# Performance work log

Hardware: AMD Instinct MI355X
Metric: run time of the kernel (lower is better)

## Reference

```python
import jax, jax.numpy as jnp
import numpy as np

B, S, D_IN, D_OUT, RANK, HBS, ABS = 4, 2048, 4096, 4096, 32, 128, 16


def _hadamard(n: int) -> np.ndarray:
    H = np.array([[1.0]], dtype=np.float64)
    while H.shape[0] < n:
        H = np.block([[H, H], [H, -H]])
    return (H / np.sqrt(n)).astype(np.float32)


def setup_inputs() -> dict:
    key = jax.random.key(0)
    ks = jax.random.split(key, 6)
    x = jax.random.normal(ks[0], (B, S, D_IN), dtype=jnp.float32)
    # random +/-1 sign vector (matches torch.randint(0,2)*2-1)
    S_in = (jax.random.randint(ks[1], (D_IN,), 0, 2) * 2 - 1).astype(jnp.float32)
    H_block = jnp.asarray(_hadamard(HBS))  # orthonormal block Hadamard
    w_quantized = jax.random.normal(ks[2], (D_OUT, D_IN), dtype=jnp.float32) * 0.02
    lora_a = jax.random.normal(ks[3], (RANK, D_IN), dtype=jnp.float32) * 0.01
    lora_b = jax.random.normal(ks[4], (D_OUT, RANK), dtype=jnp.float32) * 0.01
    bias = jax.random.normal(ks[5], (D_OUT,), dtype=jnp.float32) * 0.01
    return {"x": x, "S_in": S_in, "H_block": H_block, "w_quantized": w_quantized,
            "lora_a": lora_a, "lora_b": lora_b, "bias": bias}


def _quantize_nvfp4(x, block_size=ABS):
    # per-block (size 16) NVFP4 fake-quant; numel here is divisible by block_size
    levels = jnp.array([0.0, 0.5, 1.0, 1.5, 2.0, 3.0, 4.0, 6.0], dtype=x.dtype)
    shape = x.shape
    xf = x.reshape(-1, block_size)
    amax = jnp.maximum(jnp.max(jnp.abs(xf), axis=-1, keepdims=True), 1e-12)
    scale = amax / 6.0
    x_norm = jnp.abs(xf) / scale
    idx = jnp.argmin(jnp.abs(x_norm[..., None] - levels), axis=-1)  # snap to grid
    xq = jnp.sign(xf) * levels[idx] * scale
    return xq.reshape(shape)


def _hadamard_rotate(x, S_in, H_block):
    # sign flip then block-diagonal Hadamard on the last dim
    shape = x.shape
    x_s = x * S_in
    x3 = x_s.reshape(*shape[:-1], shape[-1] // HBS, HBS)
    return (x3 @ H_block).reshape(shape)


def reference(x, S_in, H_block, w_quantized, lora_a, lora_b, bias):
    x_rot = _hadamard_rotate(x, S_in, H_block)          # [B,S,D_IN]
    x_q = _quantize_nvfp4(x_rot)                        # NVFP4 fake-quant activations
    out = jnp.einsum('bsd,od->bso', x_q, w_quantized)   # main GEMM
    # LoRA correction on the (unquantized) rotated activations
    out = out + jnp.einsum('bsr,or->bso', jnp.einsum('bsd,rd->bsr', x_rot, lora_a), lora_b)
    out = out + bias
    return out
```

## Files before the change

kernel.cpp:

```cpp
#include <hip/hip_runtime.h>

#define M_ROWS 8192
#define DIN    4096
#define DOUT   4096
#define RANK   32
#define KAUG   4128
#define KPAD   4160
#define KTILES 65
#define ROWS_PB 4
#define NROTB  (M_ROWS / ROWS_PB)

typedef __attribute__((ext_vector_type(8))) short short8;
typedef __attribute__((ext_vector_type(4))) float floatx4;

__device__ __forceinline__ unsigned short f2bf(float f) {
    unsigned int u = __float_as_uint(f);
    unsigned int r = (u + 0x7FFFu + ((u >> 16) & 1u)) >> 16;
    return (unsigned short)r;
}

__global__ __launch_bounds__(256) void prep_kernel(
    const float* __restrict__ x, const float* __restrict__ sgn,
    const float* __restrict__ lora_a,
    const float* __restrict__ w, const float* __restrict__ lora_b,
    unsigned short* __restrict__ xaug, unsigned short* __restrict__ waug)
{
    __shared__ unsigned short xrot[ROWS_PB][DIN];
    __shared__ float tred[ROWS_PB][RANK][8];

    const int t = threadIdx.x;

    if (blockIdx.x >= NROTB) {
        const int n = blockIdx.x - NROTB;
        unsigned short* wr = waug + (size_t)n * KPAD;
        const float* wsrc = w + (size_t)n * DIN;
        #pragma unroll
        for (int it = 0; it < 2; ++it) {
            const int base = (it * 256 + t) * 8;
            float4 a = ((const float4*)wsrc)[base >> 2];
            float4 b = ((const float4*)wsrc)[(base >> 2) + 1];
            unsigned int p0 = (unsigned int)f2bf(a.x) | ((unsigned int)f2bf(a.y) << 16);
            unsigned int p1 = (unsigned int)f2bf(a.z) | ((unsigned int)f2bf(a.w) << 16);
            unsigned int p2 = (unsigned int)f2bf(b.x) | ((unsigned int)f2bf(b.y) << 16);
            unsigned int p3 = (unsigned int)f2bf(b.z) | ((unsigned int)f2bf(b.w) << 16);
            *(uint4*)(wr + base) = make_uint4(p0, p1, p2, p3);
        }
        if (t < RANK)
            wr[DIN + t] = f2bf(lora_b[(size_t)n * RANK + t]);
        if (t < 4)
            *(uint4*)&wr[KAUG + t * 8] = make_uint4(0, 0, 0, 0);
        return;
    }

    const int row0 = blockIdx.x * ROWS_PB;
    const float inv = 0.08838834764831845f;

    float sg[16];
    #pragma unroll
    for (int q = 0; q < 4; ++q)
        *(float4*)&sg[4 * q] = ((const float4*)sgn)[t * 4 + q];

    if (t < ROWS_PB * 4) {
        const int rr = t >> 2, q = t & 3;
        *(uint4*)&xaug[(size_t)(row0 + rr) * KPAD + KAUG + q * 8] =
            make_uint4(0, 0, 0, 0);
    }

    #pragma unroll 1
    for (int rr = 0; rr < ROWS_PB; ++rr) {
        const float* xr = x + (size_t)(row0 + rr) * DIN;
        float v[16];
        #pragma unroll
        for (int q = 0; q < 4; ++q)
            *(float4*)&v[4 * q] = ((const float4*)xr)[t * 4 + q];
        #pragma unroll
        for (int j = 0; j < 16; ++j) v[j] *= sg[j];

        #pragma unroll
        for (int h = 1; h < 16; h <<= 1) {
            #pragma unroll
            for (int i = 0; i < 16; ++i) {
                if (!(i & h)) {
                    float a = v[i], b = v[i + h];
                    v[i] = a + b;
                    v[i + h] = a - b;
                }
            }
        }
        #pragma unroll
        for (int m = 1; m <= 4; m <<= 1) {
            const bool up = (t & m) != 0;
            #pragma unroll
            for (int j = 0; j < 16; ++j) {
                float o = __shfl_xor(v[j], m, 64);
                v[j] = up ? (o - v[j]) : (v[j] + o);
            }
        }
        #pragma unroll
        for (int j = 0; j < 16; ++j) v[j] *= inv;

        {
            unsigned int xp[8];
            #pragma unroll
            for (int j = 0; j < 8; ++j)
                xp[j] = (unsigned int)f2bf(v[2 * j]) |
                        ((unsigned int)f2bf(v[2 * j + 1]) << 16);
            *(uint4*)&xrot[rr][16 * t]     = make_uint4(xp[0], xp[1], xp[2], xp[3]);
            *(uint4*)&xrot[rr][16 * t + 8] = make_uint4(xp[4], xp[5], xp[6], xp[7]);
        }

        {
            float amax = 0.f;
            #pragma unroll
            for (int j = 0; j < 16; ++j) amax = fmaxf(amax, fabsf(v[j]));
            amax = fmaxf(amax, 1e-12f);
            float scale = amax / 6.0f;
            unsigned int pk[8];
            #pragma unroll
            for (int j = 0; j < 8; ++j) {
                unsigned short q2[2];
                #pragma unroll
                for (int e = 0; e < 2; ++e) {
                    float vv = v[2 * j + e];
                    float an = fabsf(vv) / scale;
                    float lev = 0.0f;
                    lev = an > 0.25f ? 0.5f : lev;
                    lev = an > 0.75f ? 1.0f : lev;
                    lev = an > 1.25f ? 1.5f : lev;
                    lev = an > 1.75f ? 2.0f : lev;
                    lev = an > 2.5f  ? 3.0f : lev;
                    lev = an > 3.5f  ? 4.0f : lev;
                    lev = an > 5.0f  ? 6.0f : lev;
                    q2[e] = f2bf(copysignf(lev * scale, vv));
                }
                pk[j] = (unsigned int)q2[0] | ((unsigned int)q2[1] << 16);
            }
            unsigned short* orow = xaug + (size_t)(row0 + rr) * KPAD + 16 * t;
            ((uint4*)orow)[0] = make_uint4(pk[0], pk[1], pk[2], pk[3]);
            ((uint4*)orow)[1] = make_uint4(pk[4], pk[5], pk[6], pk[7]);
        }
    }
    __syncthreads();

    {
        const int r = t >> 3, c = t & 7;
        const float* ar = lora_a + (size_t)r * DIN;
        float acc4[ROWS_PB] = {0.f, 0.f, 0.f, 0.f};
        #pragma unroll 1
        for (int i = 0; i < 64; ++i) {
            const int d = (c << 9) + (((i << 3) + (c << 3)) & 511);
            float4 a0 = *(const float4*)(ar + d);
            float4 a1 = *(const float4*)(ar + d + 4);
            #pragma unroll
            for (int rr = 0; rr < ROWS_PB; ++rr) {
                uint4 xb = *(const uint4*)&xrot[rr][d];
                float x0 = __uint_as_float(xb.x << 16);
                float x1 = __uint_as_float(xb.x & 0xFFFF0000u);
                float x2 = __uint_as_float(xb.y << 16);
                float x3 = __uint_as_float(xb.y & 0xFFFF0000u);
                float x4 = __uint_as_float(xb.z << 16);
                float x5 = __uint_as_float(xb.z & 0xFFFF0000u);
                float x6 = __uint_as_float(xb.w << 16);
                float x7 = __uint_as_float(xb.w & 0xFFFF0000u);
                acc4[rr] += a0.x * x0 + a0.y * x1 + a0.z * x2 + a0.w * x3 +
                            a1.x * x4 + a1.y * x5 + a1.z * x6 + a1.w * x7;
            }
        }
        #pragma unroll
        for (int rr = 0; rr < ROWS_PB; ++rr) tred[rr][r][c] = acc4[rr];
    }
    __syncthreads();
    if (t < ROWS_PB * RANK) {
        const int rr = t >> 5, rk = t & 31;
        float s = 0.f;
        #pragma unroll
        for (int k = 0; k < 8; ++k) s += tred[rr][rk][k];
        xaug[(size_t)(row0 + rr) * KPAD + DIN + rk] = f2bf(s);
    }
}

__global__ __launch_bounds__(512) void gemm_kernel(
    const unsigned short* __restrict__ A,
    const unsigned short* __restrict__ Bm,
    const float* __restrict__ bias,
    float* __restrict__ C)
{
    __shared__ unsigned short As[2][2][8192];
    __shared__ unsigned short Bs[2][2][8192];

    const int bid = blockIdx.x;
    const int mt = bid >> 4, nt = bid & 15;
    const int m0 = mt * 256, n0 = nt * 256;
    const int t = threadIdx.x;
    const int wave = t >> 6, lane = t & 63;
    const int wm = wave >> 2, wn = wave & 3;
    const int lm = lane & 15, lq = lane >> 4;

    const int pr = lane >> 2;
    const int sgs = (lane & 3) ^ ((pr >> 1) & 3);
    const int cc0 = wave * 2, cc1 = wave * 2 + 1;

    const int rdo = lm * 64 + ((lq ^ ((lm >> 1) & 3)) << 4);

#define STG(MAT, RB, DST, KT, KH, CC) do {                                    \
    const unsigned short* g_ = (MAT) + (size_t)((RB) + (CC) * 16 + pr) * KPAD \
                               + (KT) * 64 + (KH) * 32 + sgs * 8;             \
    __builtin_amdgcn_global_load_lds(                                         \
        (const __attribute__((address_space(1))) void*)g_,                    \
        (__attribute__((address_space(3))) void*)((DST) + (CC) * 512),        \
        16, 0, 0); } while (0)

    floatx4 acc[8][4] = {};

    STG(A,  m0, &As[0][0][0], 0, 0, cc0); STG(A,  m0, &As[0][0][0], 0, 0, cc1);
    STG(Bm, n0, &Bs[0][0][0], 0, 0, cc0); STG(Bm, n0, &Bs[0][0][0], 0, 0, cc1);
    STG(A,  m0, &As[0][1][0], 0, 1, cc0); STG(A,  m0, &As[0][1][0], 0, 1, cc1);
    STG(Bm, n0, &Bs[0][1][0], 0, 1, cc0); STG(Bm, n0, &Bs[0][1][0], 0, 1, cc1);
    asm volatile("s_waitcnt vmcnt(4)" ::: "memory");
    __builtin_amdgcn_s_barrier();

    #pragma unroll 1
    for (int kt = 0; kt < KTILES; ++kt) {
        const int b = kt & 1;
        const bool st = (kt + 1 < KTILES);
        const char* a0c = (const char*)&As[b][0][0];
        const char* a1c = (const char*)&As[b][1][0];
        const char* b0c = (const char*)&Bs[b][0][0];
        const char* b1c = (const char*)&Bs[b][1][0];
        unsigned short* nA0 = &As[b ^ 1][0][0];
        unsigned short* nA1 = &As[b ^ 1][1][0];
        unsigned short* nB0 = &Bs[b ^ 1][0][0];
        unsigned short* nB1 = &Bs[b ^ 1][1][0];
        short8 af[4], bf[4];

        #pragma unroll
        for (int i = 0; i < 4; ++i)
            af[i] = *(const short8*)(a0c + (wm * 8 + i) * 1024 + rdo);
        #pragma unroll
        for (int j = 0; j < 4; ++j)
            bf[j] = *(const short8*)(b0c + (wn * 4 + j) * 1024 + rdo);
        if (st) { STG(A, m0, nA0, kt + 1, 0, cc0); STG(A, m0, nA0, kt + 1, 0, cc1); }
        __builtin_amdgcn_sched_barrier(0);
        __builtin_amdgcn_s_barrier();
        __builtin_amdgcn_sched_barrier(0);
        __builtin_amdgcn_s_setprio(1);
        #pragma unroll
        for (int i = 0; i < 4; ++i)
            #pragma unroll
            for (int j = 0; j < 4; ++j)
                acc[i][j] = __builtin_amdgcn_mfma_f32_16x16x32_bf16(
                    af[i], bf[j], acc[i][j], 0, 0, 0);
        __builtin_amdgcn_s_setprio(0);
        __builtin_amdgcn_sched_barrier(0);
        __builtin_amdgcn_s_barrier();

        #pragma unroll
        for (int i = 0; i < 4; ++i)
            af[i] = *(const short8*)(a0c + (wm * 8 + 4 + i) * 1024 + rdo);
        if (st) {
            STG(Bm, n0, nB0, kt + 1, 0, cc0); STG(Bm, n0, nB0, kt + 1, 0, cc1);
            asm volatile("s_waitcnt vmcnt(4)" ::: "memory");
        } else {
            asm volatile("s_waitcnt vmcnt(0)" ::: "memory");
        }
        __builtin_amdgcn_sched_barrier(0);
        __builtin_amdgcn_s_barrier();
        __builtin_amdgcn_sched_barrier(0);
        __builtin_amdgcn_s_setprio(1);
        #pragma unroll
        for (int i = 0; i < 4; ++i)
            #pragma unroll
            for (int j = 0; j < 4; ++j)
                acc[i + 4][j] = __builtin_amdgcn_mfma_f32_16x16x32_bf16(
                    af[i], bf[j], acc[i + 4][j], 0, 0, 0);
        __builtin_amdgcn_s_setprio(0);
        __builtin_amdgcn_sched_barrier(0);
        __builtin_amdgcn_s_barrier();

        #pragma unroll
        for (int i = 0; i < 4; ++i)
            af[i] = *(const short8*)(a1c + (wm * 8 + i) * 1024 + rdo);
        #pragma unroll
        for (int j = 0; j < 4; ++j)
            bf[j] = *(const short8*)(b1c + (wn * 4 + j) * 1024 + rdo);
        if (st) { STG(A, m0, nA1, kt + 1, 1, cc0); STG(A, m0, nA1, kt + 1, 1, cc1); }
        __builtin_amdgcn_sched_barrier(0);
        __builtin_amdgcn_s_barrier();
        __builtin_amdgcn_sched_barrier(0);
        __builtin_amdgcn_s_setprio(1);
        #pragma unroll
        for (int i = 0; i < 4; ++i)
            #pragma unroll
            for (int j = 0; j < 4; ++j)
                acc[i][j] = __builtin_amdgcn_mfma_f32_16x16x32_bf16(
                    af[i], bf[j], acc[i][j], 0, 0, 0);
        __builtin_amdgcn_s_setprio(0);
        __builtin_amdgcn_sched_barrier(0);
        __builtin_amdgcn_s_barrier();

        #pragma unroll
        for (int i = 0; i < 4; ++i)
            af[i] = *(const short8*)(a1c + (wm * 8 + 4 + i) * 1024 + rdo);
        if (st) {
            STG(Bm, n0, nB1, kt + 1, 1, cc0); STG(Bm, n0, nB1, kt + 1, 1, cc1);
            asm volatile("s_waitcnt vmcnt(4)" ::: "memory");
        }
        __builtin_amdgcn_sched_barrier(0);
        __builtin_amdgcn_s_barrier();
        __builtin_amdgcn_sched_barrier(0);
        __builtin_amdgcn_s_setprio(1);
        #pragma unroll
        for (int i = 0; i < 4; ++i)
            #pragma unroll
            for (int j = 0; j < 4; ++j)
                acc[i + 4][j] = __builtin_amdgcn_mfma_f32_16x16x32_bf16(
                    af[i], bf[j], acc[i + 4][j], 0, 0, 0);
        __builtin_amdgcn_s_setprio(0);
        __builtin_amdgcn_sched_barrier(0);
        __builtin_amdgcn_s_barrier();
    }
#undef STG

    float bv[4];
    #pragma unroll
    for (int j = 0; j < 4; ++j)
        bv[j] = bias[n0 + wn * 64 + j * 16 + lm];
    #pragma unroll
    for (int i = 0; i < 8; ++i) {
        #pragma unroll
        for (int j = 0; j < 4; ++j) {
            const int col = n0 + wn * 64 + j * 16 + lm;
            #pragma unroll
            for (int r = 0; r < 4; ++r) {
                const int row = m0 + wm * 128 + i * 16 + lq * 4 + r;
                C[(size_t)row * DOUT + col] = acc[i][j][r] + bv[j];
            }
        }
    }
}

extern "C" void kernel_launch(void* const* d_in, const int* in_sizes, int n_in,
                              void* d_out, int out_size, void* d_ws, size_t ws_size,
                              hipStream_t stream) {
    const float* x      = (const float*)d_in[0];
    const float* sgn    = (const float*)d_in[1];
    const float* w      = (const float*)d_in[3];
    const float* lora_a = (const float*)d_in[4];
    const float* lora_b = (const float*)d_in[5];
    const float* bias   = (const float*)d_in[6];
    float* out = (float*)d_out;

    unsigned short* xaug = (unsigned short*)d_ws;
    unsigned short* waug = xaug + (size_t)M_ROWS * KPAD;

    prep_kernel<<<NROTB + DOUT, 256, 0, stream>>>(x, sgn, lora_a, w, lora_b,
                                                  xaug, waug);
    gemm_kernel<<<(M_ROWS / 256) * (DOUT / 256), 512, 0, stream>>>(xaug, waug, bias, out);
}
```

Before: 650.1 us.

## Software-pipeline LDS fragment reads ahead of MFMA blocks with double register buffers

Restructures the GEMM main loop so the LDS fragment reads for the next MFMA sub-block are issued before the current sub-block's MFMAs, using two A and two B register fragment sets. The next tile's first fragments are prefetched at the end of each iteration. This is meant to hide LDS read latency behind matrix-core work rather than stalling before each MFMA group. In exchange it raises VGPR pressure and depends on the barrier placement being correct for the double-buffered LDS.

```diff
diff --git a/kernel.cpp b/kernel.cpp
--- a/kernel.cpp
+++ b/kernel.cpp
@@ -210,7 +210,32 @@
         (__attribute__((address_space(3))) void*)((DST) + (CC) * 512),        \
         16, 0, 0); } while (0)
 
+#define RD_A(DSTF, AD, MI0) do {                                              \
+    _Pragma("unroll")                                                         \
+    for (int i_ = 0; i_ < 4; ++i_)                                            \
+        DSTF[i_] = *(const short8*)((AD) + (wm * 8 + (MI0) + i_) * 1024 + rdo); \
+    } while (0)
+#define RD_B(DSTF, BD) do {                                                   \
+    _Pragma("unroll")                                                         \
+    for (int j_ = 0; j_ < 4; ++j_)                                            \
+        DSTF[j_] = *(const short8*)((BD) + (wn * 4 + j_) * 1024 + rdo);       \
+    } while (0)
+
+#define MM(AO, AF, BF) do {                                                   \
+    __builtin_amdgcn_s_setprio(1);                                            \
+    _Pragma("unroll")                                                         \
+    for (int i_ = 0; i_ < 4; ++i_)                                            \
+        _Pragma("unroll")                                                     \
+        for (int j_ = 0; j_ < 4; ++j_)                                        \
+            acc[(AO) + i_][j_] = __builtin_amdgcn_mfma_f32_16x16x32_bf16(     \
+                AF[i_], BF[j_], acc[(AO) + i_][j_], 0, 0, 0);                 \
+    __builtin_amdgcn_s_setprio(0);                                            \
+    } while (0)
+
+#define SBAR __builtin_amdgcn_sched_barrier(0)
+
     floatx4 acc[8][4] = {};
+    short8 afX[4], afY[4], bf0[4], bf1[4];
 
     STG(A,  m0, &As[0][0][0], 0, 0, cc0); STG(A,  m0, &As[0][0][0], 0, 0, cc1);
     STG(Bm, n0, &Bs[0][0][0], 0, 0, cc0); STG(Bm, n0, &Bs[0][0][0], 0, 0, cc1);
@@ -218,6 +243,8 @@
     STG(Bm, n0, &Bs[0][1][0], 0, 1, cc0); STG(Bm, n0, &Bs[0][1][0], 0, 1, cc1);
     asm volatile("s_waitcnt vmcnt(4)" ::: "memory");
     __builtin_amdgcn_s_barrier();
+    RD_A(afX, (const char*)&As[0][0][0], 0);
+    RD_B(bf0, (const char*)&Bs[0][0][0]);
 
     #pragma unroll 1
     for (int kt = 0; kt < KTILES; ++kt) {
@@ -225,101 +252,59 @@
         const bool st = (kt + 1 < KTILES);
         const char* a0c = (const char*)&As[b][0][0];
         const char* a1c = (const char*)&As[b][1][0];
-        const char* b0c = (const char*)&Bs[b][0][0];
         const char* b1c = (const char*)&Bs[b][1][0];
+        const char* na0 = (const char*)&As[b ^ 1][0][0];
+        const char* nb0 = (const char*)&Bs[b ^ 1][0][0];
         unsigned short* nA0 = &As[b ^ 1][0][0];
         unsigned short* nA1 = &As[b ^ 1][1][0];
         unsigned short* nB0 = &Bs[b ^ 1][0][0];
         unsigned short* nB1 = &Bs[b ^ 1][1][0];
-        short8 af[4], bf[4];
-
-        #pragma unroll
-        for (int i = 0; i < 4; ++i)
-            af[i] = *(const short8*)(a0c + (wm * 8 + i) * 1024 + rdo);
-        #pragma unroll
-        for (int j = 0; j < 4; ++j)
-            bf[j] = *(const short8*)(b0c + (wn * 4 + j) * 1024 + rdo);
+
         if (st) { STG(A, m0, nA0, kt + 1, 0, cc0); STG(A, m0, nA0, kt + 1, 0, cc1); }
-        __builtin_amdgcn_sched_barrier(0);
-        __builtin_amdgcn_s_barrier();
-        __builtin_amdgcn_sched_barrier(0);
-        __builtin_amdgcn_s_setprio(1);
-        #pragma unroll
-        for (int i = 0; i < 4; ++i)
-            #pragma unroll
-            for (int j = 0; j < 4; ++j)
-                acc[i][j] = __builtin_amdgcn_mfma_f32_16x16x32_bf16(
-                    af[i], bf[j], acc[i][j], 0, 0, 0);
-        __builtin_amdgcn_s_setprio(0);
-        __builtin_amdgcn_sched_barrier(0);
-        __builtin_amdgcn_s_barrier();
-
-        #pragma unroll
-        for (int i = 0; i < 4; ++i)
-            af[i] = *(const short8*)(a0c + (wm * 8 + 4 + i) * 1024 + rdo);
+        SBAR; __builtin_amdgcn_s_barrier(); SBAR;
+        RD_A(afY, a0c, 4);
+        SBAR;
+        MM(0, afX, bf0);
+        SBAR; __builtin_amdgcn_s_barrier();
+
         if (st) {
             STG(Bm, n0, nB0, kt + 1, 0, cc0); STG(Bm, n0, nB0, kt + 1, 0, cc1);
             asm volatile("s_waitcnt vmcnt(4)" ::: "memory");
         } else {
             asm volatile("s_waitcnt vmcnt(0)" ::: "memory");
         }
-        __builtin_amdgcn_sched_barrier(0);
-        __builtin_amdgcn_s_barrier();
-        __builtin_amdgcn_sched_barrier(0);
-        __builtin_amdgcn_s_setprio(1);
-        #pragma unroll
-        for (int i = 0; i < 4; ++i)
-            #pragma unroll
-            for (int j = 0; j < 4; ++j)
-                acc[i + 4][j] = __builtin_amdgcn_mfma_f32_16x16x32_bf16(
-                    af[i], bf[j], acc[i + 4][j], 0, 0, 0);
-        __builtin_amdgcn_s_setprio(0);
-        __builtin_amdgcn_sched_barrier(0);
-        __builtin_amdgcn_s_barrier();
-
-        #pragma unroll
-        for (int i = 0; i < 4; ++i)
-            af[i] = *(const short8*)(a1c + (wm * 8 + i) * 1024 + rdo);
-        #pragma unroll
-        for (int j = 0; j < 4; ++j)
-            bf[j] = *(const short8*)(b1c + (wn * 4 + j) * 1024 + rdo);
+        SBAR; __builtin_amdgcn_s_barrier(); SBAR;
+        RD_A(afX, a1c, 0);
+        RD_B(bf1, b1c);
+        SBAR;
+        MM(4, afY, bf0);
+        SBAR; __builtin_amdgcn_s_barrier();
+
         if (st) { STG(A, m0, nA1, kt + 1, 1, cc0); STG(A, m0, nA1, kt + 1, 1, cc1); }
-        __builtin_amdgcn_sched_barrier(0);
-        __builtin_amdgcn_s_barrier();
-        __builtin_amdgcn_sched_barrier(0);
-        __builtin_amdgcn_s_setprio(1);
-        #pragma unroll
-        for (int i = 0; i < 4; ++i)
-            #pragma unroll
-            for (int j = 0; j < 4; ++j)
-                acc[i][j] = __builtin_amdgcn_mfma_f32_16x16x32_bf16(
-                    af[i], bf[j], acc[i][j], 0, 0, 0);
-        __builtin_amdgcn_s_setprio(0);
-        __builtin_amdgcn_sched_barrier(0);
-        __builtin_amdgcn_s_barrier();
-
-        #pragma unroll
-        for (int i = 0; i < 4; ++i)
-            af[i] = *(const short8*)(a1c + (wm * 8 + 4 + i) * 1024 + rdo);
+        SBAR; __builtin_amdgcn_s_barrier(); SBAR;
+        RD_A(afY, a1c, 4);
+        SBAR;
+        MM(0, afX, bf1);
+        SBAR; __builtin_amdgcn_s_barrier();
+
         if (st) {
             STG(Bm, n0, nB1, kt + 1, 1, cc0); STG(Bm, n0, nB1, kt + 1, 1, cc1);
             asm volatile("s_waitcnt vmcnt(4)" ::: "memory");
         }
-        __builtin_amdgcn_sched_barrier(0);
-        __builtin_amdgcn_s_barrier();
-        __builtin_amdgcn_sched_barrier(0);
-        __builtin_amdgcn_s_setprio(1);
-        #pragma unroll
-        for (int i = 0; i < 4; ++i)
-            #pragma unroll
-            for (int j = 0; j < 4; ++j)
-                acc[i + 4][j] = __builtin_amdgcn_mfma_f32_16x16x32_bf16(
-                    af[i], bf[j], acc[i + 4][j], 0, 0, 0);
-        __builtin_amdgcn_s_setprio(0);
-        __builtin_amdgcn_sched_barrier(0);
-        __builtin_amdgcn_s_barrier();
+        SBAR; __builtin_amdgcn_s_barrier(); SBAR;
+        if (st) {
+            RD_A(afX, na0, 0);
+            RD_B(bf0, nb0);
+        }
+        SBAR;
+        MM(4, afY, bf1);
+        SBAR; __builtin_amdgcn_s_barrier();
     }
 #undef STG
+#undef RD_A
+#undef RD_B
+#undef MM
+#undef SBAR
 
     float bv[4];
     #pragma unroll
```

Measured after the change: 722.2 us. +11.1%, slower.
